# Kernel optimization log

Measured on AMD Instinct MI355X. Metric: run time of the kernel, lower is better.

Reference implementation:

```python
import jax, jax.numpy as jnp
import numpy as np

B, S, D = 4, 2048, 1024
NEG_BIG = -1.0e9


def setup_inputs() -> dict:
    key = jax.random.key(0)
    ks = jax.random.split(key, 9)
    scale = 1.0 / np.sqrt(D)
    inp = {
        "v": jax.random.normal(ks[0], (B, S, D), dtype=jnp.float32),
        "k": jax.random.normal(ks[1], (B, S, D), dtype=jnp.float32),
        "q": jax.random.normal(ks[2], (B, S, D), dtype=jnp.float32),
        # causal mask: 1 where attention is disallowed (j > i), broadcast over batch
        "mask": jnp.triu(jnp.ones((1, S, S), dtype=jnp.float32), k=1),
        "Wq": jax.random.normal(ks[3], (D, D), dtype=jnp.float32) * scale,
        "bq": jnp.zeros((D,), dtype=jnp.float32),
        "Wk": jax.random.normal(ks[4], (D, D), dtype=jnp.float32) * scale,
        "bk": jnp.zeros((D,), dtype=jnp.float32),
        "Wv": jax.random.normal(ks[5], (D, D), dtype=jnp.float32) * scale,
        "bv": jnp.zeros((D,), dtype=jnp.float32),
    }
    return inp


def reference(v, k, q, mask, Wq, bq, Wk, bk, Wv, bv):
    # Dense projections (Keras Dense: x @ W + b)
    qp = q @ Wq + bq  # [B, S, D]
    kp = k @ Wk + bk  # [B, S, D]
    vp = v @ Wv + bv  # [B, S, D]

    dk = jnp.asarray(D, dtype=qp.dtype)
    logits = jnp.einsum("bqd,bkd->bqk", qp, kp) / jnp.sqrt(dk)  # [B, S, S]
    logits = logits + mask * NEG_BIG
    attn = jax.nn.softmax(logits, axis=-1)  # [B, S, S]
    out = jnp.einsum("bqk,bkd->bqd", attn, vp)  # [B, S, D]
    return out, attn
```

## Files before the change

### kernel.cpp

```cpp
#include <hip/hip_runtime.h>
#include <hip/hip_bf16.h>
#include <cstdint>

#define BATCH 4
#define S_LEN 2048
#define D_DIM 1024

typedef __attribute__((ext_vector_type(4))) float f32x4_t;
typedef __attribute__((ext_vector_type(8))) __bf16 bf16x8_t;

__device__ __forceinline__ ushort f32_to_bf16(float f) {
    uint32_t u = __float_as_uint(f);
    uint32_t r = (u + 0x7FFFu + ((u >> 16) & 1u)) >> 16;
    return (ushort)r;
}

__global__ __launch_bounds__(256)
void cvt3_kernel(const float* __restrict__ a, const float* __restrict__ b,
                 const float* __restrict__ c, ushort* __restrict__ out, int n4) {
    int z = blockIdx.y;
    const float* src = (z == 0) ? a : ((z == 1) ? b : c);
    ushort* dst = out + (size_t)z * n4 * 4;
    int idx = blockIdx.x * blockDim.x + threadIdx.x;
    int stride = gridDim.x * blockDim.x;
    const float4* in4 = (const float4*)src;
    ushort4* out4 = (ushort4*)dst;
    for (int i = idx; i < n4; i += stride) {
        float4 v = in4[i];
        ushort4 o;
        o.x = f32_to_bf16(v.x);
        o.y = f32_to_bf16(v.y);
        o.z = f32_to_bf16(v.z);
        o.w = f32_to_bf16(v.w);
        out4[i] = o;
    }
}

__global__ __launch_bounds__(256)
void transpose_cvt_kernel(const float* __restrict__ in, ushort* __restrict__ out,
                          int rows, int cols) {
    __shared__ ushort tile[64][66];
    int r0 = blockIdx.y * 64, c0 = blockIdx.x * 64;
    int t = threadIdx.x;
    int cr = t & 63;
    int cc = t >> 6;
    #pragma unroll
    for (int i = 0; i < 16; ++i) {
        int r = cc * 16 + i;
        tile[r][cr] = f32_to_bf16(in[(size_t)(r0 + r) * cols + (c0 + cr)]);
    }
    __syncthreads();
    #pragma unroll
    for (int i = 0; i < 16; ++i) {
        int c = cc * 16 + i;
        out[(size_t)(c0 + c) * rows + (r0 + cr)] = tile[cr][c];
    }
}

__global__ __launch_bounds__(256)
void transpose_bf16_kernel(const ushort* __restrict__ in, ushort* __restrict__ out,
                           int rows, int cols, int lda, long strideA, long strideB) {
    __shared__ ushort tile[64][66];
    const ushort* src = in + (size_t)blockIdx.z * strideA;
    ushort* dst = out + (size_t)blockIdx.z * strideB;
    int r0 = blockIdx.y * 64, c0 = blockIdx.x * 64;
    int t = threadIdx.x;
    int cr = t & 63;
    int cc = t >> 6;
    #pragma unroll
    for (int i = 0; i < 16; ++i) {
        int r = cc * 16 + i;
        tile[r][cr] = src[(size_t)(r0 + r) * lda + (c0 + cr)];
    }
    __syncthreads();
    #pragma unroll
    for (int i = 0; i < 16; ++i) {
        int c = cc * 16 + i;
        dst[(size_t)(c0 + c) * rows + (r0 + cr)] = tile[cr][c];
    }
}

enum { MODE_PROJ = 0, MODE_LOGITS = 1, MODE_OUT = 2 };

#define GBM 128
#define GBN 128
#define GBK 32

template<int MODE>
__global__ __launch_bounds__(256)
void gemm_bt_kernel(const ushort* __restrict__ A, const ushort* __restrict__ Bt,
                    const float* __restrict__ bias, void* __restrict__ Cout,
                    int K, int lda, int ldb, int ldc,
                    long strideA, long strideB, long strideC, float scale) {
    int bc = blockIdx.x, br = blockIdx.y, bz = blockIdx.z;
    if (MODE == MODE_LOGITS && bc > br) return;

    __shared__ ushort As[2][GBM * GBK];
    __shared__ ushort Bs[2][GBN * GBK];

    const ushort* Ab = (MODE == MODE_PROJ) ? A + (size_t)(bc >> 3) * strideA
                                           : A + (size_t)bz * strideA;
    const ushort* Bb = Bt + (size_t)bz * strideB;

    int brow = br * GBM, bcol = bc * GBN;
    int t = threadIdx.x;
    int lane = t & 63;
    int wave = t >> 6;
    int wr = wave >> 1, wc = wave & 1;

    int ksteps = K / GBK;
    if (MODE == MODE_OUT) ksteps = min(ksteps, (brow + GBM) / GBK);

    f32x4_t acc[4][4];
    #pragma unroll
    for (int m = 0; m < 4; ++m)
        #pragma unroll
        for (int n = 0; n < 4; ++n)
            acc[m][n] = (f32x4_t){0.f, 0.f, 0.f, 0.f};

    int row0 = t >> 2;
    int col0 = (t & 3) * 8;

    auto stage = [&](int kt, int buf) {
        int k0 = kt * GBK;
        #pragma unroll
        for (int i = 0; i < 2; ++i) {
            int row = i * 64 + row0;
            const ushort* srcA = Ab + (size_t)(brow + row) * lda + (k0 + col0);
            __builtin_amdgcn_global_load_lds(
                (const __attribute__((address_space(1))) uint32_t*)srcA,
                (__attribute__((address_space(3))) uint32_t*)&As[buf][(i * 256 + t) * 8],
                16, 0, 0);
            const ushort* srcB = Bb + (size_t)(bcol + row) * ldb + (k0 + col0);
            __builtin_amdgcn_global_load_lds(
                (const __attribute__((address_space(1))) uint32_t*)srcB,
                (__attribute__((address_space(3))) uint32_t*)&Bs[buf][(i * 256 + t) * 8],
                16, 0, 0);
        }
    };

    stage(0, 0);
    __syncthreads();

    for (int kt = 0; kt < ksteps; ++kt) {
        int cur = kt & 1;
        if (kt + 1 < ksteps) stage(kt + 1, cur ^ 1);

        bf16x8_t a_frag[4], b_frag[4];
        int arow = wr * 64 + (lane & 15);
        int kcol = (lane >> 4) * 8;
        #pragma unroll
        for (int m = 0; m < 4; ++m)
            a_frag[m] = *(const bf16x8_t*)&As[cur][(arow + m * 16) * GBK + kcol];
        int brl = wc * 64 + (lane & 15);
        #pragma unroll
        for (int n = 0; n < 4; ++n)
            b_frag[n] = *(const bf16x8_t*)&Bs[cur][(brl + n * 16) * GBK + kcol];

        __builtin_amdgcn_s_setprio(1);
        #pragma unroll
        for (int m = 0; m < 4; ++m)
            #pragma unroll
            for (int n = 0; n < 4; ++n)
                acc[m][n] = __builtin_amdgcn_mfma_f32_16x16x32_bf16(
                    a_frag[m], b_frag[n], acc[m][n], 0, 0, 0);
        __builtin_amdgcn_s_setprio(0);

        __syncthreads();
    }

    int crow0 = brow + wr * 64 + ((lane >> 4) * 4);
    int ccol0 = bcol + wc * 64 + (lane & 15);
    if (MODE == MODE_PROJ) {
        ushort* C = (ushort*)Cout;
        #pragma unroll
        for (int m = 0; m < 4; ++m) {
            #pragma unroll
            for (int n = 0; n < 4; ++n) {
                int col = ccol0 + n * 16;
                float bv = bias[col];
                #pragma unroll
                for (int j = 0; j < 4; ++j) {
                    int rowg = crow0 + m * 16 + j;
                    C[(size_t)rowg * ldc + col] = f32_to_bf16(acc[m][n][j] + bv);
                }
            }
        }
    } else {
        float* C = (float*)Cout + (size_t)bz * strideC;
        #pragma unroll
        for (int m = 0; m < 4; ++m)
            #pragma unroll
            for (int n = 0; n < 4; ++n) {
                int col = ccol0 + n * 16;
                #pragma unroll
                for (int j = 0; j < 4; ++j) {
                    int rowg = crow0 + m * 16 + j;
                    C[(size_t)rowg * ldc + col] = acc[m][n][j] * scale;
                }
            }
    }
}

__global__ __launch_bounds__(256)
void bias_concat_kernel(const float* __restrict__ bq, const float* __restrict__ bk,
                        const float* __restrict__ bv, float* __restrict__ out) {
    int i = blockIdx.x * blockDim.x + threadIdx.x;
    if (i < D_DIM) out[i] = bq[i];
    else if (i < 2 * D_DIM) out[i] = bk[i - D_DIM];
    else if (i < 3 * D_DIM) out[i] = bv[i - 2 * D_DIM];
}

__global__ __launch_bounds__(256)
void softmax_causal_kernel(float* __restrict__ attn, ushort* __restrict__ attn_bf) {
    int rowid = blockIdx.x;
    int i = rowid & (S_LEN - 1);
    float* lrow = attn + (size_t)rowid * S_LEN;
    ushort* brw = attn_bf + (size_t)rowid * S_LEN;
    int t = threadIdx.x;
    int nvalid = i + 1;

    float vals[8];
    float lmax = -1e30f;
    #pragma unroll
    for (int it = 0; it < 8; ++it) {
        int j = it * 256 + t;
        float v = (j < nvalid) ? lrow[j] : -1e30f;
        vals[it] = v;
        lmax = fmaxf(lmax, v);
    }
    #pragma unroll
    for (int off = 32; off > 0; off >>= 1)
        lmax = fmaxf(lmax, __shfl_xor(lmax, off));

    __shared__ float redm[4];
    __shared__ float reds[4];
    int wave = t >> 6, lane = t & 63;
    if (lane == 0) redm[wave] = lmax;
    __syncthreads();
    float m = fmaxf(fmaxf(redm[0], redm[1]), fmaxf(redm[2], redm[3]));

    float lsum = 0.f;
    #pragma unroll
    for (int it = 0; it < 8; ++it) {
        int j = it * 256 + t;
        float e = (j < nvalid) ? __expf(vals[it] - m) : 0.f;
        vals[it] = e;
        lsum += e;
    }
    #pragma unroll
    for (int off = 32; off > 0; off >>= 1)
        lsum += __shfl_xor(lsum, off);
    if (lane == 0) reds[wave] = lsum;
    __syncthreads();
    float denom = reds[0] + reds[1] + reds[2] + reds[3];
    float inv = 1.f / denom;

    #pragma unroll
    for (int it = 0; it < 8; ++it) {
        int j = it * 256 + t;
        float p = vals[it] * inv;
        lrow[j] = p;
        brw[j] = f32_to_bf16(p);
    }
}

extern "C" void kernel_launch(void* const* d_in, const int* in_sizes, int n_in,
                              void* d_out, int out_size, void* d_ws, size_t ws_size,
                              hipStream_t stream) {
    const float* v  = (const float*)d_in[0];
    const float* k  = (const float*)d_in[1];
    const float* q  = (const float*)d_in[2];
    const float* Wq = (const float*)d_in[4];
    const float* bq = (const float*)d_in[5];
    const float* Wk = (const float*)d_in[6];
    const float* bk = (const float*)d_in[7];
    const float* Wv = (const float*)d_in[8];
    const float* bv = (const float*)d_in[9];

    float* out  = (float*)d_out;
    float* attn = (float*)d_out + (size_t)BATCH * S_LEN * D_DIM;

    char* ws = (char*)d_ws;
    const size_t NTOK = (size_t)BATCH * S_LEN;
    const size_t XSZ  = NTOK * D_DIM * sizeof(ushort);
    ushort* xqkv  = (ushort*)(ws);
    ushort* qkvp  = (ushort*)(ws + 3 * XSZ);
    ushort* WT    = (ushort*)(ws + 6 * XSZ);
    float*  bias3 = (float*)(ws + 6 * XSZ + 3 * (size_t)D_DIM * D_DIM * sizeof(ushort));
    ushort* vpT     = (ushort*)(ws);
    ushort* attn_bf = (ushort*)(ws + XSZ);

    const int n4 = (int)(NTOK * D_DIM / 4);
    cvt3_kernel<<<dim3(1024, 3), dim3(256), 0, stream>>>(q, k, v, xqkv, n4);

    transpose_cvt_kernel<<<dim3(16, 16), dim3(256), 0, stream>>>(Wq, WT, D_DIM, D_DIM);
    transpose_cvt_kernel<<<dim3(16, 16), dim3(256), 0, stream>>>(Wk, WT + (size_t)D_DIM * D_DIM, D_DIM, D_DIM);
    transpose_cvt_kernel<<<dim3(16, 16), dim3(256), 0, stream>>>(Wv, WT + 2 * (size_t)D_DIM * D_DIM, D_DIM, D_DIM);
    bias_concat_kernel<<<dim3(12), dim3(256), 0, stream>>>(bq, bk, bv, bias3);

    dim3 pgrid(3 * D_DIM / GBN, (int)(NTOK / GBM), 1);
    gemm_bt_kernel<MODE_PROJ><<<pgrid, dim3(256), 0, stream>>>(
        xqkv, WT, bias3, qkvp, D_DIM, D_DIM, D_DIM, 3 * D_DIM,
        (long)NTOK * D_DIM, 0, 0, 1.f);

    transpose_bf16_kernel<<<dim3(D_DIM / 64, S_LEN / 64, BATCH), dim3(256), 0, stream>>>(
        qkvp + 2 * D_DIM, vpT, S_LEN, D_DIM, 3 * D_DIM,
        (long)S_LEN * 3 * D_DIM, (long)D_DIM * S_LEN);

    dim3 lgrid(S_LEN / GBN, S_LEN / GBM, BATCH);
    gemm_bt_kernel<MODE_LOGITS><<<lgrid, dim3(256), 0, stream>>>(
        qkvp, qkvp + D_DIM, nullptr, attn, D_DIM, 3 * D_DIM, 3 * D_DIM, S_LEN,
        (long)S_LEN * 3 * D_DIM, (long)S_LEN * 3 * D_DIM, (long)S_LEN * S_LEN, 0.03125f);

    softmax_causal_kernel<<<dim3((int)NTOK), dim3(256), 0, stream>>>(attn, attn_bf);

    dim3 ogrid(D_DIM / GBN, S_LEN / GBM, BATCH);
    gemm_bt_kernel<MODE_OUT><<<ogrid, dim3(256), 0, stream>>>(
        attn_bf, vpT, nullptr, out, S_LEN, S_LEN, S_LEN, D_DIM,
        (long)S_LEN * S_LEN, (long)D_DIM * S_LEN, (long)S_LEN * D_DIM, 1.f);
}
```

Baseline: 243.1 us.

## Fold Wq·Wkᵀ into one matrix, fuse V transpose, retile GEMMs with triple buffering

Precomputes M = Wq·Wkᵀ so logits become (q·M)·kᵀ, removing the separate K projection. The key-bias term is dropped as row-constant and the query-bias term becomes a per-key vector added in softmax. The V projection now writes its output already transposed, so the separate transpose kernel goes away. The GEMM moves to 128x256 tiles with 512 threads, a 3-stage LDS pipeline with vmcnt gating, XOR-swizzled LDS and an XCD-aware block swizzle. Softmax skips fully masked chunks and writes zeros there, at the cost of a different rounding order for the logits.

```diff
diff --git a/kernel.cpp b/kernel.cpp
--- a/kernel.cpp
+++ b/kernel.cpp
@@ -37,6 +37,27 @@
 }
 
 __global__ __launch_bounds__(256)
+void cvt2_kernel(const float* __restrict__ a, const float* __restrict__ b,
+                 ushort* __restrict__ out, int n4) {
+    int z = blockIdx.y;
+    const float* src = (z == 0) ? a : b;
+    ushort* dst = out + (size_t)z * n4 * 4;
+    int idx = blockIdx.x * blockDim.x + threadIdx.x;
+    int stride = gridDim.x * blockDim.x;
+    const float4* in4 = (const float4*)src;
+    ushort4* out4 = (ushort4*)dst;
+    for (int i = idx; i < n4; i += stride) {
+        float4 v = in4[i];
+        ushort4 o;
+        o.x = f32_to_bf16(v.x);
+        o.y = f32_to_bf16(v.y);
+        o.z = f32_to_bf16(v.z);
+        o.w = f32_to_bf16(v.w);
+        out4[i] = o;
+    }
+}
+
+__global__ __launch_bounds__(256)
 void transpose_cvt_kernel(const float* __restrict__ in, ushort* __restrict__ out,
                           int rows, int cols) {
     __shared__ ushort tile[64][66];
@@ -58,58 +79,130 @@
 }
 
 __global__ __launch_bounds__(256)
-void transpose_bf16_kernel(const ushort* __restrict__ in, ushort* __restrict__ out,
-                           int rows, int cols, int lda, long strideA, long strideB) {
-    __shared__ ushort tile[64][66];
-    const ushort* src = in + (size_t)blockIdx.z * strideA;
-    ushort* dst = out + (size_t)blockIdx.z * strideB;
-    int r0 = blockIdx.y * 64, c0 = blockIdx.x * 64;
-    int t = threadIdx.x;
-    int cr = t & 63;
-    int cc = t >> 6;
-    #pragma unroll
-    for (int i = 0; i < 16; ++i) {
-        int r = cc * 16 + i;
-        tile[r][cr] = src[(size_t)(r0 + r) * lda + (c0 + cr)];
-    }
-    __syncthreads();
-    #pragma unroll
-    for (int i = 0; i < 16; ++i) {
-        int c = cc * 16 + i;
-        dst[(size_t)(c0 + c) * rows + (r0 + cr)] = tile[cr][c];
-    }
-}
-
-enum { MODE_PROJ = 0, MODE_LOGITS = 1, MODE_OUT = 2 };
-
-#define GBM 128
-#define GBN 128
-#define GBK 32
+void fill_kernel(const float* __restrict__ bv, float* __restrict__ bias2,
+                 float* __restrict__ zb) {
+    int i = blockIdx.x * blockDim.x + threadIdx.x;
+    bias2[i] = (i < D_DIM) ? 0.f : bv[i - D_DIM];
+    zb[i] = 0.f;
+}
+
+__global__ __launch_bounds__(256)
+void hv_kernel(const float* __restrict__ Wk, const float* __restrict__ bq,
+               float* __restrict__ hv) {
+    int wave = threadIdx.x >> 6, lane = threadIdx.x & 63;
+    int r = blockIdx.x * 4 + wave;
+    const float* row = Wk + (size_t)r * D_DIM;
+    float s = 0.f;
+    #pragma unroll
+    for (int it = 0; it < 16; ++it)
+        s += row[it * 64 + lane] * bq[it * 64 + lane];
+    #pragma unroll
+    for (int off = 32; off > 0; off >>= 1)
+        s += __shfl_xor(s, off);
+    if (lane == 0) hv[r] = s;
+}
+
+__global__ __launch_bounds__(256)
+void wvec_kernel(const ushort* __restrict__ xk, const float* __restrict__ hv,
+                 float* __restrict__ w) {
+    int wave = threadIdx.x >> 6, lane = threadIdx.x & 63;
+    int r = blockIdx.x * 4 + wave;
+    const ushort* row = xk + (size_t)r * D_DIM + lane * 16;
+    const float* hp = hv + lane * 16;
+    float s = 0.f;
+    #pragma unroll
+    for (int it = 0; it < 16; ++it) {
+        uint32_t u = row[it];
+        s += __uint_as_float(u << 16) * hp[it];
+    }
+    #pragma unroll
+    for (int off = 32; off > 0; off >>= 1)
+        s += __shfl_xor(s, off);
+    if (lane == 0) w[r] = s * 0.03125f;
+}
+
+enum { MODE_PROJ = 0, MODE_MT = 1, MODE_LOGITS = 2, MODE_OUT = 3 };
+
+#define GATE(N) do { asm volatile("s_waitcnt vmcnt(" #N ")" ::: "memory"); \
+    __builtin_amdgcn_sched_barrier(0); } while (0)
+#define GLOAD(dst, src) __builtin_amdgcn_global_load_lds( \
+    (const __attribute__((address_space(1))) uint32_t*)(src), \
+    (__attribute__((address_space(3))) uint32_t*)(dst), 16, 0, 0)
+
+__device__ __forceinline__ void xcd_swizzle(int& bc, int& br) {
+    int gx = gridDim.x;
+    int nwg = gx * gridDim.y;
+    int orig = blockIdx.y * gx + blockIdx.x;
+    int xcd = orig & 7, idx = orig >> 3;
+    int wgid = xcd * (nwg >> 3) + idx;
+    bc = wgid % gx;
+    br = wgid / gx;
+}
 
 template<int MODE>
-__global__ __launch_bounds__(256)
-void gemm_bt_kernel(const ushort* __restrict__ A, const ushort* __restrict__ Bt,
-                    const float* __restrict__ bias, void* __restrict__ Cout,
-                    int K, int lda, int ldb, int ldc,
-                    long strideA, long strideB, long strideC, float scale) {
-    int bc = blockIdx.x, br = blockIdx.y, bz = blockIdx.z;
-    if (MODE == MODE_LOGITS && bc > br) return;
-
-    __shared__ ushort As[2][GBM * GBK];
-    __shared__ ushort Bs[2][GBN * GBK];
-
-    const ushort* Ab = (MODE == MODE_PROJ) ? A + (size_t)(bc >> 3) * strideA
+__global__ __launch_bounds__(512, 4)
+void gemm_t_kernel(const ushort* __restrict__ A, const ushort* __restrict__ Bt,
+                   const float* __restrict__ bias, void* __restrict__ Cout,
+                   ushort* __restrict__ vpTp,
+                   int nkt0, int lda, int ldb, int ldc,
+                   long strideA, long strideB, long strideC, float scale) {
+    __shared__ ushort As[3][128 * 32];
+    __shared__ ushort Bs[3][256 * 32];
+    int bc, br;
+    xcd_swizzle(bc, br);
+    int bz = blockIdx.z;
+    if (MODE == MODE_LOGITS && 2 * bc > br) return;
+    const ushort* Ab = (MODE == MODE_PROJ) ? A + (size_t)((bc >> 2) * 2) * strideA
                                            : A + (size_t)bz * strideA;
     const ushort* Bb = Bt + (size_t)bz * strideB;
-
-    int brow = br * GBM, bcol = bc * GBN;
-    int t = threadIdx.x;
-    int lane = t & 63;
-    int wave = t >> 6;
-    int wr = wave >> 1, wc = wave & 1;
-
-    int ksteps = K / GBK;
-    if (MODE == MODE_OUT) ksteps = min(ksteps, (brow + GBM) / GBK);
+    int brow = br * 128, bcol = bc * 256;
+    int t = threadIdx.x, lane = t & 63, wid = t >> 6;
+    int wr = wid >> 2, wc = wid & 3;
+    int nkt = nkt0;
+    if (MODE == MODE_OUT) nkt = min(nkt, (brow + 128) / 32);
+
+    int oA, oB0, oB1;
+    const ushort* aS;
+    const ushort* bS0;
+    const ushort* bS1;
+    {
+        int o = t * 16;
+        int row = o >> 6;
+        int colb = (o & 63) ^ ((row & 3) << 4);
+        oA = o >> 1;
+        aS = Ab + (size_t)(brow + row) * lda + (colb >> 1);
+    }
+    {
+        int o = t * 16;
+        int row = o >> 6;
+        int colb = (o & 63) ^ ((row & 3) << 4);
+        oB0 = o >> 1;
+        bS0 = Bb + (size_t)(bcol + row) * ldb + (colb >> 1);
+        o = (512 + t) * 16;
+        row = o >> 6;
+        colb = (o & 63) ^ ((row & 3) << 4);
+        oB1 = o >> 1;
+        bS1 = Bb + (size_t)(bcol + row) * ldb + (colb >> 1);
+    }
+    auto stage = [&](int tk, int slot) {
+        GLOAD(&As[slot][0] + oA, aS + tk * 32);
+        GLOAD(&Bs[slot][0] + oB0, bS0 + tk * 32);
+        GLOAD(&Bs[slot][0] + oB1, bS1 + tk * 32);
+    };
+
+    int rdA[4], rdB[4];
+    #pragma unroll
+    for (int m = 0; m < 4; ++m) {
+        int ra = wr * 64 + m * 16 + (lane & 15);
+        int cb = (lane >> 4) * 16;
+        rdA[m] = ra * 64 + (cb ^ ((ra & 3) << 4));
+    }
+    #pragma unroll
+    for (int n = 0; n < 4; ++n) {
+        int rb = wc * 64 + n * 16 + (lane & 15);
+        int cb = (lane >> 4) * 16;
+        rdB[n] = rb * 64 + (cb ^ ((rb & 3) << 4));
+    }
 
     f32x4_t acc[4][4];
     #pragma unroll
@@ -118,44 +211,23 @@
         for (int n = 0; n < 4; ++n)
             acc[m][n] = (f32x4_t){0.f, 0.f, 0.f, 0.f};
 
-    int row0 = t >> 2;
-    int col0 = (t & 3) * 8;
-
-    auto stage = [&](int kt, int buf) {
-        int k0 = kt * GBK;
-        #pragma unroll
-        for (int i = 0; i < 2; ++i) {
-            int row = i * 64 + row0;
-            const ushort* srcA = Ab + (size_t)(brow + row) * lda + (k0 + col0);
-            __builtin_amdgcn_global_load_lds(
-                (const __attribute__((address_space(1))) uint32_t*)srcA,
-                (__attribute__((address_space(3))) uint32_t*)&As[buf][(i * 256 + t) * 8],
-                16, 0, 0);
-            const ushort* srcB = Bb + (size_t)(bcol + row) * ldb + (k0 + col0);
-            __builtin_amdgcn_global_load_lds(
-                (const __attribute__((address_space(1))) uint32_t*)srcB,
-                (__attribute__((address_space(3))) uint32_t*)&Bs[buf][(i * 256 + t) * 8],
-                16, 0, 0);
-        }
-    };
-
     stage(0, 0);
-    __syncthreads();
-
-    for (int kt = 0; kt < ksteps; ++kt) {
-        int cur = kt & 1;
-        if (kt + 1 < ksteps) stage(kt + 1, cur ^ 1);
-
-        bf16x8_t a_frag[4], b_frag[4];
-        int arow = wr * 64 + (lane & 15);
-        int kcol = (lane >> 4) * 8;
-        #pragma unroll
-        for (int m = 0; m < 4; ++m)
-            a_frag[m] = *(const bf16x8_t*)&As[cur][(arow + m * 16) * GBK + kcol];
-        int brl = wc * 64 + (lane & 15);
-        #pragma unroll
-        for (int n = 0; n < 4; ++n)
-            b_frag[n] = *(const bf16x8_t*)&Bs[cur][(brl + n * 16) * GBK + kcol];
+    stage(1, 1);
+    GATE(3);
+    __builtin_amdgcn_s_barrier();
+
+    for (int kt = 0; kt < nkt; ++kt) {
+        int cur = kt % 3;
+        int s2 = kt + 2 < nkt ? (kt + 2) % 3 : 0;
+        if (kt + 2 < nkt) stage(kt + 2, s2);
+
+        const char* bA = (const char*)&As[cur][0];
+        const char* bB = (const char*)&Bs[cur][0];
+        bf16x8_t af[4], bf[4];
+        #pragma unroll
+        for (int m = 0; m < 4; ++m) af[m] = *(const bf16x8_t*)(bA + rdA[m]);
+        #pragma unroll
+        for (int n = 0; n < 4; ++n) bf[n] = *(const bf16x8_t*)(bB + rdB[n]);
 
         __builtin_amdgcn_s_setprio(1);
         #pragma unroll
@@ -163,71 +235,92 @@
             #pragma unroll
             for (int n = 0; n < 4; ++n)
                 acc[m][n] = __builtin_amdgcn_mfma_f32_16x16x32_bf16(
-                    a_frag[m], b_frag[n], acc[m][n], 0, 0, 0);
+                    af[m], bf[n], acc[m][n], 0, 0, 0);
         __builtin_amdgcn_s_setprio(0);
 
-        __syncthreads();
+        if (kt + 1 < nkt) {
+            if (kt + 2 < nkt) { GATE(3); }
+            else              { GATE(0); }
+        }
+        __builtin_amdgcn_s_barrier();
     }
 
     int crow0 = brow + wr * 64 + ((lane >> 4) * 4);
     int ccol0 = bcol + wc * 64 + (lane & 15);
     if (MODE == MODE_PROJ) {
-        ushort* C = (ushort*)Cout;
-        #pragma unroll
-        for (int m = 0; m < 4; ++m) {
+        #pragma unroll
+        for (int mf = 0; mf < 4; ++mf) {
             #pragma unroll
-            for (int n = 0; n < 4; ++n) {
-                int col = ccol0 + n * 16;
-                float bv = bias[col];
-                #pragma unroll
-                for (int j = 0; j < 4; ++j) {
-                    int rowg = crow0 + m * 16 + j;
-                    C[(size_t)rowg * ldc + col] = f32_to_bf16(acc[m][n][j] + bv);
+            for (int nf = 0; nf < 4; ++nf) {
+                int gcol = ccol0 + nf * 16;
+                float bv = bias[gcol];
+                int rowg = crow0 + mf * 16;
+                if (gcol < D_DIM) {
+                    ushort* C = (ushort*)Cout;
+                    #pragma unroll
+                    for (int j = 0; j < 4; ++j)
+                        C[(size_t)(rowg + j) * D_DIM + gcol] = f32_to_bf16(acc[mf][nf][j] + bv);
+                } else {
+                    int d = gcol - D_DIM;
+                    int b = rowg >> 11, s = rowg & 2047;
+                    ushort4 o;
+                    o.x = f32_to_bf16(acc[mf][nf][0] + bv);
+                    o.y = f32_to_bf16(acc[mf][nf][1] + bv);
+                    o.z = f32_to_bf16(acc[mf][nf][2] + bv);
+                    o.w = f32_to_bf16(acc[mf][nf][3] + bv);
+                    *(ushort4*)&vpTp[((size_t)b * D_DIM + d) * S_LEN + s] = o;
                 }
             }
         }
+    } else if (MODE == MODE_MT) {
+        ushort* C = (ushort*)Cout;
+        #pragma unroll
+        for (int mf = 0; mf < 4; ++mf)
+            #pragma unroll
+            for (int nf = 0; nf < 4; ++nf) {
+                int gcol = ccol0 + nf * 16;
+                int rowg = crow0 + mf * 16;
+                #pragma unroll
+                for (int j = 0; j < 4; ++j)
+                    C[(size_t)(rowg + j) * ldc + gcol] = f32_to_bf16(acc[mf][nf][j]);
+            }
     } else {
         float* C = (float*)Cout + (size_t)bz * strideC;
         #pragma unroll
-        for (int m = 0; m < 4; ++m)
+        for (int mf = 0; mf < 4; ++mf)
             #pragma unroll
-            for (int n = 0; n < 4; ++n) {
-                int col = ccol0 + n * 16;
+            for (int nf = 0; nf < 4; ++nf) {
+                int gcol = ccol0 + nf * 16;
+                int rowg = crow0 + mf * 16;
                 #pragma unroll
-                for (int j = 0; j < 4; ++j) {
-                    int rowg = crow0 + m * 16 + j;
-                    C[(size_t)rowg * ldc + col] = acc[m][n][j] * scale;
-                }
+                for (int j = 0; j < 4; ++j)
+                    C[(size_t)(rowg + j) * ldc + gcol] = acc[mf][nf][j] * scale;
             }
     }
 }
 
 __global__ __launch_bounds__(256)
-void bias_concat_kernel(const float* __restrict__ bq, const float* __restrict__ bk,
-                        const float* __restrict__ bv, float* __restrict__ out) {
-    int i = blockIdx.x * blockDim.x + threadIdx.x;
-    if (i < D_DIM) out[i] = bq[i];
-    else if (i < 2 * D_DIM) out[i] = bk[i - D_DIM];
-    else if (i < 3 * D_DIM) out[i] = bv[i - 2 * D_DIM];
-}
-
-__global__ __launch_bounds__(256)
-void softmax_causal_kernel(float* __restrict__ attn, ushort* __restrict__ attn_bf) {
+void softmax_causal_kernel(float* __restrict__ attn, ushort* __restrict__ attn_bf,
+                           const float* __restrict__ w) {
     int rowid = blockIdx.x;
     int i = rowid & (S_LEN - 1);
     float* lrow = attn + (size_t)rowid * S_LEN;
     ushort* brw = attn_bf + (size_t)rowid * S_LEN;
+    const float* wv = w + (rowid & ~(S_LEN - 1));
     int t = threadIdx.x;
     int nvalid = i + 1;
+    int nact = (nvalid + 255) >> 8;
 
     float vals[8];
     float lmax = -1e30f;
     #pragma unroll
     for (int it = 0; it < 8; ++it) {
-        int j = it * 256 + t;
-        float v = (j < nvalid) ? lrow[j] : -1e30f;
-        vals[it] = v;
-        lmax = fmaxf(lmax, v);
+        if (it < nact) {
+            int j = it * 256 + t;
+            float v = (j < nvalid) ? (lrow[j] + wv[j]) : -1e30f;
+            vals[it] = v;
+            lmax = fmaxf(lmax, v);
+        }
     }
     #pragma unroll
     for (int off = 32; off > 0; off >>= 1)
@@ -243,10 +336,12 @@
     float lsum = 0.f;
     #pragma unroll
     for (int it = 0; it < 8; ++it) {
-        int j = it * 256 + t;
-        float e = (j < nvalid) ? __expf(vals[it] - m) : 0.f;
-        vals[it] = e;
-        lsum += e;
+        if (it < nact) {
+            int j = it * 256 + t;
+            float e = (j < nvalid) ? __expf(vals[it] - m) : 0.f;
+            vals[it] = e;
+            lsum += e;
+        }
     }
     #pragma unroll
     for (int off = 32; off > 0; off >>= 1)
@@ -259,9 +354,13 @@
     #pragma unroll
     for (int it = 0; it < 8; ++it) {
         int j = it * 256 + t;
-        float p = vals[it] * inv;
-        lrow[j] = p;
-        brw[j] = f32_to_bf16(p);
+        if (it < nact) {
+            float p = vals[it] * inv;
+            lrow[j] = p;
+            brw[j] = f32_to_bf16(p);
+        } else {
+            lrow[j] = 0.f;
+        }
     }
 }
 
@@ -282,41 +381,46 @@
     float* attn = (float*)d_out + (size_t)BATCH * S_LEN * D_DIM;
 
     char* ws = (char*)d_ws;
+    const size_t MB = 1024u * 1024u;
     const size_t NTOK = (size_t)BATCH * S_LEN;
-    const size_t XSZ  = NTOK * D_DIM * sizeof(ushort);
     ushort* xqkv  = (ushort*)(ws);
-    ushort* qkvp  = (ushort*)(ws + 3 * XSZ);
-    ushort* WT    = (ushort*)(ws + 6 * XSZ);
-    float*  bias3 = (float*)(ws + 6 * XSZ + 3 * (size_t)D_DIM * D_DIM * sizeof(ushort));
-    ushort* vpT     = (ushort*)(ws);
-    ushort* attn_bf = (ushort*)(ws + XSZ);
+    ushort* xq    = xqkv;
+    ushort* xk    = xqkv + NTOK * D_DIM;
+    ushort* qq    = (ushort*)(ws + 48 * MB);
+    ushort* vpT   = (ushort*)(ws + 64 * MB);
+    ushort* Btp   = (ushort*)(ws + 80 * MB);
+    ushort* xW    = (ushort*)(ws + 84 * MB);
+    float*  bias2 = (float*)(ws + 88 * MB);
+    float*  zb    = (float*)(ws + 88 * MB + 8192);
+    float*  hvb   = (float*)(ws + 88 * MB + 16384);
+    float*  wvec  = (float*)(ws + 88 * MB + 20480);
+    ushort* attn_bf = (ushort*)(ws);
 
     const int n4 = (int)(NTOK * D_DIM / 4);
     cvt3_kernel<<<dim3(1024, 3), dim3(256), 0, stream>>>(q, k, v, xqkv, n4);
-
-    transpose_cvt_kernel<<<dim3(16, 16), dim3(256), 0, stream>>>(Wq, WT, D_DIM, D_DIM);
-    transpose_cvt_kernel<<<dim3(16, 16), dim3(256), 0, stream>>>(Wk, WT + (size_t)D_DIM * D_DIM, D_DIM, D_DIM);
-    transpose_cvt_kernel<<<dim3(16, 16), dim3(256), 0, stream>>>(Wv, WT + 2 * (size_t)D_DIM * D_DIM, D_DIM, D_DIM);
-    bias_concat_kernel<<<dim3(12), dim3(256), 0, stream>>>(bq, bk, bv, bias3);
-
-    dim3 pgrid(3 * D_DIM / GBN, (int)(NTOK / GBM), 1);
-    gemm_bt_kernel<MODE_PROJ><<<pgrid, dim3(256), 0, stream>>>(
-        xqkv, WT, bias3, qkvp, D_DIM, D_DIM, D_DIM, 3 * D_DIM,
-        (long)NTOK * D_DIM, 0, 0, 1.f);
-
-    transpose_bf16_kernel<<<dim3(D_DIM / 64, S_LEN / 64, BATCH), dim3(256), 0, stream>>>(
-        qkvp + 2 * D_DIM, vpT, S_LEN, D_DIM, 3 * D_DIM,
-        (long)S_LEN * 3 * D_DIM, (long)D_DIM * S_LEN);
-
-    dim3 lgrid(S_LEN / GBN, S_LEN / GBM, BATCH);
-    gemm_bt_kernel<MODE_LOGITS><<<lgrid, dim3(256), 0, stream>>>(
-        qkvp, qkvp + D_DIM, nullptr, attn, D_DIM, 3 * D_DIM, 3 * D_DIM, S_LEN,
-        (long)S_LEN * 3 * D_DIM, (long)S_LEN * 3 * D_DIM, (long)S_LEN * S_LEN, 0.03125f);
-
-    softmax_causal_kernel<<<dim3((int)NTOK), dim3(256), 0, stream>>>(attn, attn_bf);
-
-    dim3 ogrid(D_DIM / GBN, S_LEN / GBM, BATCH);
-    gemm_bt_kernel<MODE_OUT><<<ogrid, dim3(256), 0, stream>>>(
-        attn_bf, vpT, nullptr, out, S_LEN, S_LEN, S_LEN, D_DIM,
+    cvt2_kernel<<<dim3(256, 2), dim3(256), 0, stream>>>(Wk, Wq, xW, D_DIM * D_DIM / 4);
+    transpose_cvt_kernel<<<dim3(16, 16), dim3(256), 0, stream>>>(Wv, Btp + (size_t)D_DIM * D_DIM, D_DIM, D_DIM);
+    fill_kernel<<<dim3(8), dim3(256), 0, stream>>>(bv, bias2, zb);
+    hv_kernel<<<dim3(256), dim3(256), 0, stream>>>(Wk, bq, hvb);
+    wvec_kernel<<<dim3(2048), dim3(256), 0, stream>>>(xk, hvb, wvec);
+
+    gemm_t_kernel<MODE_MT><<<dim3(4, 8, 1), dim3(512), 0, stream>>>(
+        xW, xW + (size_t)D_DIM * D_DIM, zb, Btp, nullptr,
+        D_DIM / 32, D_DIM, D_DIM, D_DIM, 0, 0, 0, 1.f);
+
+    gemm_t_kernel<MODE_PROJ><<<dim3(8, 64, 1), dim3(512), 0, stream>>>(
+        xqkv, Btp, bias2, qq, vpT,
+        D_DIM / 32, D_DIM, D_DIM, D_DIM, (long)NTOK * D_DIM, 0, 0, 1.f);
+
+    gemm_t_kernel<MODE_LOGITS><<<dim3(8, 16, BATCH), dim3(512), 0, stream>>>(
+        qq, xk, nullptr, attn, nullptr,
+        D_DIM / 32, D_DIM, D_DIM, S_LEN,
+        (long)S_LEN * D_DIM, (long)S_LEN * D_DIM, (long)S_LEN * S_LEN, 0.03125f);
+
+    softmax_causal_kernel<<<dim3((int)NTOK), dim3(256), 0, stream>>>(attn, attn_bf, wvec);
+
+    gemm_t_kernel<MODE_OUT><<<dim3(4, 16, BATCH), dim3(512), 0, stream>>>(
+        attn_bf, vpT, nullptr, out, nullptr,
+        S_LEN / 32, S_LEN, S_LEN, D_DIM,
         (long)S_LEN * S_LEN, (long)D_DIM * S_LEN, (long)S_LEN * D_DIM, 1.f);
 }
```

Result: faster. 238.1 us (-2.0%).
